# Performance work log

Hardware: AMD Instinct MI355X
Metric: run time of the kernel (lower is better)

Reference implementation:

```python
import jax, jax.numpy as jnp
import numpy as np

N_USERS = 100000
N_ITEMS = 50000
N_NODES = N_USERS + N_ITEMS
EMB_DIM = 64
N_EDGES = 4000000
N_LAYERS = 3
BATCH = 4096


def setup_inputs() -> dict:
    key = jax.random.key(0)
    k = jax.random.split(key, 7)
    return {
        "user_emb": jax.random.normal(k[0], (N_USERS, EMB_DIM), dtype=jnp.float32) * 0.1,
        "item_emb": jax.random.normal(k[1], (N_ITEMS, EMB_DIM), dtype=jnp.float32) * 0.1,
        "vals": jax.random.uniform(k[2], (N_EDGES,), dtype=jnp.float32),
        "src": jax.random.randint(k[3], (N_EDGES,), 0, N_NODES, dtype=jnp.int32),
        "dst": jax.random.randint(k[4], (N_EDGES,), 0, N_NODES, dtype=jnp.int32),
        "users": jax.random.randint(k[5], (BATCH,), 0, N_USERS, dtype=jnp.int32),
        "items": jax.random.randint(k[6], (BATCH,), 0, N_ITEMS, dtype=jnp.int32),
    }


def _propagate(user_emb, item_emb, vals, src, dst):
    # all_emb: [N, D]; sparse adjacency A given as COO (src -> dst, weight vals)
    all_emb = jnp.concatenate([user_emb, item_emb], axis=0)
    acc = all_emb  # running sum over layers (layer 0 included)
    emb = all_emb
    for _ in range(N_LAYERS):
        # SpMM: out[d] = sum_{e: dst[e]==d} vals[e] * emb[src[e]]
        msgs = vals[:, None] * emb[src]               # [E, D]
        emb = jax.ops.segment_sum(msgs, dst, num_segments=N_NODES)
        acc = acc + emb
    light_out = acc / jnp.float32(N_LAYERS + 1)       # mean over stacked layers
    return light_out[:N_USERS], light_out[N_USERS:]


def reference(user_emb, item_emb, vals, src, dst, users, items):
    all_users, all_items = _propagate(user_emb, item_emb, vals, src, dst)
    u = all_users[users]                              # [B, D]
    i = all_items[items]                              # [B, D]
    gamma = jnp.sum(u * i, axis=1)                    # [B]
    return gamma
```

## Files before the change

kernel.cpp:

```cpp
#include <hip/hip_runtime.h>
#include <hip/hip_bf16.h>

#define N_USERS 100000
#define N_ITEMS 50000
#define N_NODES 150000
#define DIM 64
#define N_EDGES 4000000
#define BATCH 4096

#define NBKT 512
#define BW 294
#define STRIDE 9216
#define PA_EDGES 4096
#define PA_ITER 16
#define SCAP 384
#define SLIST_CAP 262144

__device__ __forceinline__ float blo(unsigned int u) { return __uint_as_float(u << 16); }
__device__ __forceinline__ float bhi(unsigned int u) { return __uint_as_float(u & 0xffff0000u); }
__device__ __forceinline__ unsigned int f2b(float f) {
    unsigned int x = __float_as_uint(f);
    return (x + 0x7fffu + ((x >> 16) & 1u)) >> 16;
}
__device__ __forceinline__ unsigned int pack2(float a, float b) {
    return f2b(a) | (f2b(b) << 16);
}

typedef float v2f __attribute__((ext_vector_type(2)));

__global__ void k_markcvt(const float* __restrict__ uemb, const float* __restrict__ iemb,
                          ushort* __restrict__ out, const int* __restrict__ users,
                          const int* __restrict__ items, int* __restrict__ map,
                          int* __restrict__ sdeg, int* __restrict__ sfill,
                          int* __restrict__ gcur, int* __restrict__ scnt) {
    int tid = blockIdx.x * blockDim.x + threadIdx.x;
    if (tid < 2 * BATCH) {
        sdeg[tid] = 0;
        sfill[tid] = 0;
        if (tid < NBKT) gcur[tid] = 0;
        if (tid == 0) scnt[0] = 0;
        if (tid < BATCH) map[users[tid]] = tid;
        else map[items[tid - BATCH] + N_USERS] = tid;
    }
    int i = tid * 4;
    if (i >= N_NODES * DIM) return;
    const float* srcp = (i < N_USERS * DIM) ? (uemb + i) : (iemb + (i - N_USERS * DIM));
    float4 v;
    v.x = __builtin_nontemporal_load(srcp + 0);
    v.y = __builtin_nontemporal_load(srcp + 1);
    v.z = __builtin_nontemporal_load(srcp + 2);
    v.w = __builtin_nontemporal_load(srcp + 3);
    *(uint2*)(out + i) = make_uint2(pack2(v.x, v.y), pack2(v.z, v.w));
}

__global__ void __launch_bounds__(256, 4) k_partition(
        const int* __restrict__ src, const int* __restrict__ dst,
        const float* __restrict__ vals, const int* __restrict__ map,
        int* __restrict__ gcur, int2* __restrict__ tmp,
        int* __restrict__ sdeg, int* __restrict__ scnt,
        unsigned long long* __restrict__ slist) {
    __shared__ int cnt[NBKT];
    __shared__ int base_s[NBKT];
    __shared__ unsigned long long sbuf[SCAP];
    __shared__ int scnt_s, sbase_s;
    int t = threadIdx.x;
    for (int i = t; i < NBKT; i += 256) cnt[i] = 0;
    if (t == 0) scnt_s = 0;
    __syncthreads();
    size_t base = (size_t)blockIdx.x * PA_EDGES;
    int myb[PA_ITER];
    int mykey[PA_ITER];
    int myval[PA_ITER];
#pragma unroll
    for (int it = 0; it < PA_ITER; it++) {
        size_t i = base + (size_t)it * 256 + t;
        myb[it] = -1;
        if (i < N_EDGES) {
            int d = __builtin_nontemporal_load(dst + i);
            int s = __builtin_nontemporal_load(src + i);
            float v = __builtin_nontemporal_load(vals + i);
            int b = d / BW;
            int local = d - b * BW;
            myb[it] = b;
            mykey[it] = (s << 9) | local;
            myval[it] = __float_as_int(v);
            atomicAdd(&cnt[b], 1);
            int ms = map[d];
            if (ms >= 0) {
                atomicAdd(&sdeg[ms], 1);
                unsigned long long pk = ((unsigned long long)(unsigned int)__float_as_int(v) << 32) |
                                        ((unsigned int)ms << 18) | (unsigned int)s;
                int sl = atomicAdd(&scnt_s, 1);
                if (sl < SCAP) sbuf[sl] = pk;
                else slist[atomicAdd(scnt, 1)] = pk;
            }
        }
    }
    __syncthreads();
    for (int i = t; i < NBKT; i += 256) {
        int c = cnt[i];
        base_s[i] = (c > 0) ? atomicAdd(&gcur[i], c) : 0;
    }
    if (t == 0) {
        int c = min(scnt_s, SCAP);
        sbase_s = (c > 0) ? atomicAdd(scnt, c) : 0;
    }
    __syncthreads();
    for (int i = t; i < NBKT; i += 256) cnt[i] = 0;
    __syncthreads();
    int stot = min(scnt_s, SCAP);
    for (int i = t; i < stot; i += 256) slist[sbase_s + i] = sbuf[i];
#pragma unroll
    for (int it = 0; it < PA_ITER; it++) {
        int b = myb[it];
        if (b >= 0) {
            int pos = base_s[b] + atomicAdd(&cnt[b], 1);
            tmp[(size_t)b * STRIDE + pos] = make_int2(mykey[it], myval[it]);
        }
    }
}

__global__ void k_scan2(const int* __restrict__ gcur, int* __restrict__ bucket_ptr,
                        const int* __restrict__ sdeg, int* __restrict__ srow) {
    __shared__ int ws[16];
    int t = threadIdx.x;
    if (blockIdx.x == 0) {
        if (t >= 64) return;
        int lane = t;
        int carry = 0;
        for (int c = 0; c < NBKT / 64; c++) {
            int i = c * 64 + lane;
            int x = gcur[i];
            int incl = x;
            for (int off = 1; off < 64; off <<= 1) {
                int y = __shfl_up(incl, off);
                if (lane >= off) incl += y;
            }
            bucket_ptr[i] = carry + incl - x;
            carry += __shfl(incl, 63);
        }
        if (lane == 0) bucket_ptr[NBKT] = N_EDGES;
        return;
    }
    int v[8], p = 0;
#pragma unroll
    for (int j = 0; j < 8; j++) { v[j] = sdeg[t * 8 + j]; p += v[j]; }
    int lane = t & 63, w = t >> 6;
    int incl = p;
    for (int o = 1; o < 64; o <<= 1) {
        int y = __shfl_up(incl, o);
        if (lane >= o) incl += y;
    }
    if (lane == 63) ws[w] = incl;
    __syncthreads();
    int woff = 0;
    for (int j = 0; j < w; j++) woff += ws[j];
    int run = woff + incl - p;
#pragma unroll
    for (int j = 0; j < 8; j++) { srow[t * 8 + j] = run; run += v[j]; }
    if (t == 1023) srow[8192] = run;
}

__global__ void k_sscatter(const unsigned long long* __restrict__ slist,
                           const int* __restrict__ scnt, const int* __restrict__ srow,
                           int* __restrict__ sfill, int2* __restrict__ sfin) {
    int i = blockIdx.x * blockDim.x + threadIdx.x;
    if (i >= scnt[0]) return;
    unsigned long long pk = slist[i];
    int s = (int)(pk & 0x3FFFFu);
    int slot = (int)((pk >> 18) & 8191u);
    int vbits = (int)(pk >> 32);
    int pos = srow[slot] + atomicAdd(&sfill[slot], 1);
    sfin[pos] = make_int2(s, vbits);
}

__global__ void k_bsort(const int2* __restrict__ tmp, const int* __restrict__ gcur,
                        const int* __restrict__ bucket_ptr, int* __restrict__ row_ptr,
                        int2* __restrict__ fin) {
    __shared__ int cnt[BW + 64];
    __shared__ int off[BW + 64];
    int b = blockIdx.x, t = threadIdx.x;
    int node0 = b * BW;
    int nodes = min(BW, N_NODES - node0);
    int gbase = bucket_ptr[b];
    int count = gcur[b];
    const int2* tb = tmp + (size_t)b * STRIDE;
    for (int i = t; i < BW + 64; i += 512) cnt[i] = 0;
    __syncthreads();
    for (int e = t; e < count; e += 512) atomicAdd(&cnt[tb[e].x & 511], 1);
    __syncthreads();
    if (t < 64) {
        int lane = t;
        int carry = 0;
        for (int c = 0; c < 5; c++) {
            int i = c * 64 + lane;
            int x = (i < nodes) ? cnt[i] : 0;
            int incl = x;
            for (int o = 1; o < 64; o <<= 1) {
                int y = __shfl_up(incl, o);
                if (lane >= o) incl += y;
            }
            if (i <= nodes) off[i] = carry + incl - x;
            carry += __shfl(incl, 63);
        }
    }
    __syncthreads();
    for (int i = t; i <= nodes; i += 512)
        if (node0 + i <= N_NODES) row_ptr[node0 + i] = gbase + off[i];
    __syncthreads();
    for (int e = t; e < count; e += 512) {
        int2 r = tb[e];
        int local = r.x & 511;
        int pos = gbase + atomicAdd(&off[local], 1);
        fin[pos] = make_int2(r.x >> 9, r.y);
    }
}


#define EDGE_FMA(r, u)                                                        \
    {                                                                         \
        float vf = __int_as_float((r).y);                                     \
        v2f vv = {vf, vf};                                                    \
        v2f f0 = {blo((u).x), bhi((u).x)};                                    \
        v2f f1 = {blo((u).y), bhi((u).y)};                                    \
        v2f f2 = {blo((u).z), bhi((u).z)};                                    \
        v2f f3 = {blo((u).w), bhi((u).w)};                                    \
        acc0 = __builtin_elementwise_fma(vv, f0, acc0);                       \
        acc1 = __builtin_elementwise_fma(vv, f1, acc1);                       \
        acc2 = __builtin_elementwise_fma(vv, f2, acc2);                       \
        acc3 = __builtin_elementwise_fma(vv, f3, acc3);                       \
    }

#define GATHER16(basec, r) (*(const uint4*)((basec) + ((((unsigned int)(r).x) << 7) | qoff)))
#define REC8(basec, i) (*(const int2*)((basec) + (((unsigned int)(i)) << 3)))

#define BURST32(basec)                                                        \
    {                                                                         \
        int e1 = e + 8, e2 = e + 16, e3 = e + 24;                             \
        int2 ra = REC8(basec, e);                                             \
        int2 rb = REC8(basec, min(e1, last));                                 \
        int2 rc = REC8(basec, min(e2, last));                                 \
        int2 rd = REC8(basec, min(e3, last));                                 \
        rb.y = (e1 < end) ? rb.y : 0;                                         \
        rc.y = (e2 < end) ? rc.y : 0;                                         \
        rd.y = (e3 < end) ? rd.y : 0;                                         \
        uint4 ua = GATHER16(einc, ra);                                        \
        uint4 ub = GATHER16(einc, rb);                                        \
        uint4 uc = GATHER16(einc, rc);                                        \
        uint4 ud = GATHER16(einc, rd);                                        \
        EDGE_FMA(ra, ua);                                                     \
        EDGE_FMA(rb, ub);                                                     \
        EDGE_FMA(rc, uc);                                                     \
        EDGE_FMA(rd, ud);                                                     \
        e += 32;                                                              \
    }

__global__ void k_spmm16(const ushort* __restrict__ ein, ushort* __restrict__ eout,
                         const int* __restrict__ row_ptr, const int2* __restrict__ fin) {
    int wave = (blockIdx.x * blockDim.x + threadIdx.x) >> 6;
    if (wave >= N_NODES) return;
    int lane = threadIdx.x & 63;
    int g = lane >> 3;
    int q = lane & 7;
    unsigned int qoff = (unsigned int)q << 4;
    const char* einc = (const char*)ein;
    const char* finc = (const char*)fin;
    int start = row_ptr[wave], end = row_ptr[wave + 1];
    int last = max(start, end - 1);
    v2f acc0 = {0.f, 0.f}, acc1 = {0.f, 0.f}, acc2 = {0.f, 0.f}, acc3 = {0.f, 0.f};
    int e = start + g;
    while (e < end) BURST32(finc);
#pragma unroll
    for (int off = 8; off < 64; off <<= 1) {
        acc0.x += __shfl_xor(acc0.x, off);
        acc0.y += __shfl_xor(acc0.y, off);
        acc1.x += __shfl_xor(acc1.x, off);
        acc1.y += __shfl_xor(acc1.y, off);
        acc2.x += __shfl_xor(acc2.x, off);
        acc2.y += __shfl_xor(acc2.y, off);
        acc3.x += __shfl_xor(acc3.x, off);
        acc3.y += __shfl_xor(acc3.y, off);
    }
    if (lane < 8) {
        uint4 p;
        p.x = pack2(acc0.x, acc0.y);
        p.y = pack2(acc1.x, acc1.y);
        p.z = pack2(acc2.x, acc2.y);
        p.w = pack2(acc3.x, acc3.y);
        *(uint4*)(eout + (size_t)wave * DIM + q * 8) = p;
    }
}

__global__ void k_samp(const ushort* __restrict__ ein, const int* __restrict__ srow,
                       const int2* __restrict__ sfin, float* __restrict__ l3) {
    int slot = (blockIdx.x * blockDim.x + threadIdx.x) >> 6;
    if (slot >= 2 * BATCH) return;
    int lane = threadIdx.x & 63;
    int g = lane >> 3;
    int q = lane & 7;
    unsigned int qoff = (unsigned int)q << 4;
    const char* einc = (const char*)ein;
    const char* sfc = (const char*)sfin;
    int start = srow[slot], end = srow[slot + 1];
    int last = max(start, end - 1);
    v2f acc0 = {0.f, 0.f}, acc1 = {0.f, 0.f}, acc2 = {0.f, 0.f}, acc3 = {0.f, 0.f};
    int e = start + g;
    while (e < end) BURST32(sfc);
#pragma unroll
    for (int off = 8; off < 64; off <<= 1) {
        acc0.x += __shfl_xor(acc0.x, off);
        acc0.y += __shfl_xor(acc0.y, off);
        acc1.x += __shfl_xor(acc1.x, off);
        acc1.y += __shfl_xor(acc1.y, off);
        acc2.x += __shfl_xor(acc2.x, off);
        acc2.y += __shfl_xor(acc2.y, off);
        acc3.x += __shfl_xor(acc3.x, off);
        acc3.y += __shfl_xor(acc3.y, off);
    }
    if (lane < 8) {
        float* row = l3 + (size_t)slot * DIM + q * 8;
        *(float4*)row = make_float4(acc0.x, acc0.y, acc1.x, acc1.y);
        *(float4*)(row + 4) = make_float4(acc2.x, acc2.y, acc3.x, acc3.y);
    }
}

__global__ void k_gacc0(const float* __restrict__ uemb, const float* __restrict__ iemb,
                        const ushort* __restrict__ emb, const int* __restrict__ users,
                        const int* __restrict__ items, float* __restrict__ accU,
                        float* __restrict__ accI) {
    int i = blockIdx.x * blockDim.x + threadIdx.x;
    if (i >= 2 * BATCH * DIM) return;
    int j = (i < BATCH * DIM) ? i : i - BATCH * DIM;
    int b = j >> 6, l = j & 63;
    if (i < BATCH * DIM) {
        int n = users[b];
        unsigned int u = emb[(size_t)n * DIM + l];
        accU[j] = uemb[(size_t)n * DIM + l] + __uint_as_float(u << 16);
    } else {
        int n = items[b];
        unsigned int u = emb[(size_t)(n + N_USERS) * DIM + l];
        accI[j] = iemb[(size_t)n * DIM + l] + __uint_as_float(u << 16);
    }
}

__global__ void k_gacc(const ushort* __restrict__ emb, const int* __restrict__ users,
                       const int* __restrict__ items, float* __restrict__ accU,
                       float* __restrict__ accI) {
    int i = blockIdx.x * blockDim.x + threadIdx.x;
    if (i >= 2 * BATCH * DIM) return;
    int j = (i < BATCH * DIM) ? i : i - BATCH * DIM;
    int b = j >> 6, l = j & 63;
    if (i < BATCH * DIM) {
        unsigned int u = emb[(size_t)users[b] * DIM + l];
        accU[j] += __uint_as_float(u << 16);
    } else {
        unsigned int u = emb[(size_t)(items[b] + N_USERS) * DIM + l];
        accI[j] += __uint_as_float(u << 16);
    }
}

__global__ void k_dot(const float* __restrict__ accU, const float* __restrict__ accI,
                      const float* __restrict__ l3, const int* __restrict__ map,
                      const int* __restrict__ users, const int* __restrict__ items,
                      float* __restrict__ out) {
    int b = (blockIdx.x * blockDim.x + threadIdx.x) >> 6;
    if (b >= BATCH) return;
    int lane = threadIdx.x & 63;
    int cu = map[users[b]];
    int ci = map[items[b] + N_USERS];
    float aU = accU[b * 64 + lane] + l3[(size_t)cu * 64 + lane];
    float aI = accI[b * 64 + lane] + l3[(size_t)ci * 64 + lane];
    float p = aU * aI;
    for (int off = 32; off; off >>= 1) p += __shfl_xor(p, off);
    if (lane == 0) out[b] = p * (1.0f / 16.0f);
}


extern "C" void kernel_launch(void* const* d_in, const int* in_sizes, int n_in,
                              void* d_out, int out_size, void* d_ws, size_t ws_size,
                              hipStream_t stream) {
    const float* user_emb = (const float*)d_in[0];
    const float* item_emb = (const float*)d_in[1];
    const float* vals = (const float*)d_in[2];
    const int* src = (const int*)d_in[3];
    const int* dst = (const int*)d_in[4];
    const int* users = (const int*)d_in[5];
    const int* items = (const int*)d_in[6];
    float* out = (float*)d_out;

    char* ws = (char*)d_ws;
    size_t off = 0;
    auto alloc = [&](size_t bytes) {
        char* p = ws + off;
        off += (bytes + 255) & ~(size_t)255;
        return p;
    };
    ushort* ebf0 = (ushort*)alloc((size_t)N_NODES * DIM * 2);
    ushort* ebf1 = (ushort*)alloc((size_t)N_NODES * DIM * 2);
    ushort* ebf2 = (ushort*)alloc((size_t)N_NODES * DIM * 2);
    int2* fin = (int2*)alloc((size_t)N_EDGES * 8);
    int* row_ptr = (int*)alloc((size_t)(N_NODES + 1) * 4);
    int* bucket_ptr = (int*)alloc((size_t)(NBKT + 1) * 4);
    int* gcur = (int*)alloc((size_t)NBKT * 4);
    int* map = (int*)alloc((size_t)N_NODES * 4);
    int* sdeg = (int*)alloc((size_t)2 * BATCH * 4);
    int* srow = (int*)alloc((size_t)(2 * BATCH + 1) * 4);
    int* sfill = (int*)alloc((size_t)2 * BATCH * 4);
    int* scnt = (int*)alloc(256);
    unsigned long long* slist = (unsigned long long*)alloc((size_t)SLIST_CAP * 8);
    int2* sfin = (int2*)alloc((size_t)SLIST_CAP * 8);
    float* l3 = (float*)alloc((size_t)2 * BATCH * DIM * 4);
    float* accU = (float*)alloc((size_t)BATCH * DIM * 4);
    float* accI = (float*)alloc((size_t)BATCH * DIM * 4);
    int2* tmp = (int2*)ebf1;

    hipMemsetAsync(map, 0xFF, (size_t)N_NODES * 4, stream);

    k_markcvt<<<(N_NODES * DIM / 4 + 255) / 256, 256, 0, stream>>>(
        user_emb, item_emb, ebf0, users, items, map, sdeg, sfill, gcur, scnt);

    int pa_blocks = (N_EDGES + PA_EDGES - 1) / PA_EDGES;
    k_partition<<<pa_blocks, 256, 0, stream>>>(src, dst, vals, map, gcur, tmp, sdeg, scnt, slist);
    k_scan2<<<2, 1024, 0, stream>>>(gcur, bucket_ptr, sdeg, srow);
    k_sscatter<<<SLIST_CAP / 256, 256, 0, stream>>>(slist, scnt, srow, sfill, sfin);
    k_bsort<<<NBKT, 512, 0, stream>>>(tmp, gcur, bucket_ptr, row_ptr, fin);

    int gb = (2 * BATCH * DIM + 255) / 256;
    int spmm_blocks = (N_NODES * 64 + 255) / 256;
    k_spmm16<<<spmm_blocks, 256, 0, stream>>>(ebf0, ebf1, row_ptr, fin);
    k_gacc0<<<gb, 256, 0, stream>>>(user_emb, item_emb, ebf1, users, items, accU, accI);
    k_spmm16<<<spmm_blocks, 256, 0, stream>>>(ebf1, ebf2, row_ptr, fin);
    k_gacc<<<gb, 256, 0, stream>>>(ebf2, users, items, accU, accI);
    k_samp<<<(2 * BATCH * 64 + 255) / 256, 256, 0, stream>>>(ebf2, srow, sfin, l3);

    k_dot<<<(BATCH * 64 + 255) / 256, 256, 0, stream>>>(accU, accI, l3, map, users, items, out);
}
```

Baseline: 382.2 us.

## Drop sampled-row side list; stage partition writes in LDS for coalesced scatter

Removes the separate map/sdeg/slist/sscatter machinery that built a private CSR for the batch's sampled nodes. The final-layer sample kernel now reads the batch rows directly from the global CSR (row_ptr/fin). This eliminates a memset, the per-edge map lookups and atomics, and two kernel launches. The partition kernel also locally sorts each block's edges by bucket in shared memory and writes them out contiguously per bucket, which should make the global scatter writes more coalesced. The cost is more LDS per block (about 45KB), which may reduce occupancy.

```diff
diff --git a/kernel.cpp b/kernel.cpp
--- a/kernel.cpp
+++ b/kernel.cpp
@@ -13,8 +13,6 @@
 #define STRIDE 9216
 #define PA_EDGES 4096
 #define PA_ITER 16
-#define SCAP 384
-#define SLIST_CAP 262144
 
 __device__ __forceinline__ float blo(unsigned int u) { return __uint_as_float(u << 16); }
 __device__ __forceinline__ float bhi(unsigned int u) { return __uint_as_float(u & 0xffff0000u); }
@@ -29,19 +27,9 @@
 typedef float v2f __attribute__((ext_vector_type(2)));
 
 __global__ void k_markcvt(const float* __restrict__ uemb, const float* __restrict__ iemb,
-                          ushort* __restrict__ out, const int* __restrict__ users,
-                          const int* __restrict__ items, int* __restrict__ map,
-                          int* __restrict__ sdeg, int* __restrict__ sfill,
-                          int* __restrict__ gcur, int* __restrict__ scnt) {
+                          ushort* __restrict__ out, int* __restrict__ gcur) {
     int tid = blockIdx.x * blockDim.x + threadIdx.x;
-    if (tid < 2 * BATCH) {
-        sdeg[tid] = 0;
-        sfill[tid] = 0;
-        if (tid < NBKT) gcur[tid] = 0;
-        if (tid == 0) scnt[0] = 0;
-        if (tid < BATCH) map[users[tid]] = tid;
-        else map[items[tid - BATCH] + N_USERS] = tid;
-    }
+    if (tid < NBKT) gcur[tid] = 0;
     int i = tid * 4;
     if (i >= N_NODES * DIM) return;
     const float* srcp = (i < N_USERS * DIM) ? (uemb + i) : (iemb + (i - N_USERS * DIM));
@@ -55,17 +43,15 @@
 
 __global__ void __launch_bounds__(256, 4) k_partition(
         const int* __restrict__ src, const int* __restrict__ dst,
-        const float* __restrict__ vals, const int* __restrict__ map,
-        int* __restrict__ gcur, int2* __restrict__ tmp,
-        int* __restrict__ sdeg, int* __restrict__ scnt,
-        unsigned long long* __restrict__ slist) {
+        const float* __restrict__ vals,
+        int* __restrict__ gcur, int2* __restrict__ tmp) {
     __shared__ int cnt[NBKT];
     __shared__ int base_s[NBKT];
-    __shared__ unsigned long long sbuf[SCAP];
-    __shared__ int scnt_s, sbase_s;
+    __shared__ int off_s[NBKT];
+    __shared__ int2 rec_s[PA_EDGES];
+    __shared__ ushort bin_s[PA_EDGES];
     int t = threadIdx.x;
     for (int i = t; i < NBKT; i += 256) cnt[i] = 0;
-    if (t == 0) scnt_s = 0;
     __syncthreads();
     size_t base = (size_t)blockIdx.x * PA_EDGES;
     int myb[PA_ITER];
@@ -85,15 +71,6 @@
             mykey[it] = (s << 9) | local;
             myval[it] = __float_as_int(v);
             atomicAdd(&cnt[b], 1);
-            int ms = map[d];
-            if (ms >= 0) {
-                atomicAdd(&sdeg[ms], 1);
-                unsigned long long pk = ((unsigned long long)(unsigned int)__float_as_int(v) << 32) |
-                                        ((unsigned int)ms << 18) | (unsigned int)s;
-                int sl = atomicAdd(&scnt_s, 1);
-                if (sl < SCAP) sbuf[sl] = pk;
-                else slist[atomicAdd(scnt, 1)] = pk;
-            }
         }
     }
     __syncthreads();
@@ -101,77 +78,57 @@
         int c = cnt[i];
         base_s[i] = (c > 0) ? atomicAdd(&gcur[i], c) : 0;
     }
-    if (t == 0) {
-        int c = min(scnt_s, SCAP);
-        sbase_s = (c > 0) ? atomicAdd(scnt, c) : 0;
+    if (t < 64) {
+        int lane = t;
+        int carry = 0;
+        for (int c = 0; c < NBKT / 64; c++) {
+            int i = c * 64 + lane;
+            int x = cnt[i];
+            int incl = x;
+            for (int o = 1; o < 64; o <<= 1) {
+                int y = __shfl_up(incl, o);
+                if (lane >= o) incl += y;
+            }
+            off_s[i] = carry + incl - x;
+            carry += __shfl(incl, 63);
+        }
     }
     __syncthreads();
     for (int i = t; i < NBKT; i += 256) cnt[i] = 0;
     __syncthreads();
-    int stot = min(scnt_s, SCAP);
-    for (int i = t; i < stot; i += 256) slist[sbase_s + i] = sbuf[i];
 #pragma unroll
     for (int it = 0; it < PA_ITER; it++) {
         int b = myb[it];
         if (b >= 0) {
-            int pos = base_s[b] + atomicAdd(&cnt[b], 1);
-            tmp[(size_t)b * STRIDE + pos] = make_int2(mykey[it], myval[it]);
-        }
-    }
-}
-
-__global__ void k_scan2(const int* __restrict__ gcur, int* __restrict__ bucket_ptr,
-                        const int* __restrict__ sdeg, int* __restrict__ srow) {
-    __shared__ int ws[16];
-    int t = threadIdx.x;
-    if (blockIdx.x == 0) {
-        if (t >= 64) return;
-        int lane = t;
-        int carry = 0;
-        for (int c = 0; c < NBKT / 64; c++) {
-            int i = c * 64 + lane;
-            int x = gcur[i];
-            int incl = x;
-            for (int off = 1; off < 64; off <<= 1) {
-                int y = __shfl_up(incl, off);
-                if (lane >= off) incl += y;
-            }
-            bucket_ptr[i] = carry + incl - x;
-            carry += __shfl(incl, 63);
-        }
-        if (lane == 0) bucket_ptr[NBKT] = N_EDGES;
-        return;
-    }
-    int v[8], p = 0;
-#pragma unroll
-    for (int j = 0; j < 8; j++) { v[j] = sdeg[t * 8 + j]; p += v[j]; }
-    int lane = t & 63, w = t >> 6;
-    int incl = p;
-    for (int o = 1; o < 64; o <<= 1) {
-        int y = __shfl_up(incl, o);
-        if (lane >= o) incl += y;
-    }
-    if (lane == 63) ws[w] = incl;
-    __syncthreads();
-    int woff = 0;
-    for (int j = 0; j < w; j++) woff += ws[j];
-    int run = woff + incl - p;
-#pragma unroll
-    for (int j = 0; j < 8; j++) { srow[t * 8 + j] = run; run += v[j]; }
-    if (t == 1023) srow[8192] = run;
-}
-
-__global__ void k_sscatter(const unsigned long long* __restrict__ slist,
-                           const int* __restrict__ scnt, const int* __restrict__ srow,
-                           int* __restrict__ sfill, int2* __restrict__ sfin) {
-    int i = blockIdx.x * blockDim.x + threadIdx.x;
-    if (i >= scnt[0]) return;
-    unsigned long long pk = slist[i];
-    int s = (int)(pk & 0x3FFFFu);
-    int slot = (int)((pk >> 18) & 8191u);
-    int vbits = (int)(pk >> 32);
-    int pos = srow[slot] + atomicAdd(&sfill[slot], 1);
-    sfin[pos] = make_int2(s, vbits);
+            int pos = off_s[b] + atomicAdd(&cnt[b], 1);
+            rec_s[pos] = make_int2(mykey[it], myval[it]);
+            bin_s[pos] = (ushort)b;
+        }
+    }
+    __syncthreads();
+    int nrec = off_s[NBKT - 1] + cnt[NBKT - 1];
+    for (int i = t; i < nrec; i += 256) {
+        int2 r = rec_s[i];
+        int b = bin_s[i];
+        tmp[(size_t)b * STRIDE + base_s[b] + (i - off_s[b])] = r;
+    }
+}
+
+__global__ void k_scan(const int* __restrict__ gcur, int* __restrict__ bucket_ptr) {
+    int lane = threadIdx.x;
+    int carry = 0;
+    for (int c = 0; c < NBKT / 64; c++) {
+        int i = c * 64 + lane;
+        int x = gcur[i];
+        int incl = x;
+        for (int off = 1; off < 64; off <<= 1) {
+            int y = __shfl_up(incl, off);
+            if (lane >= off) incl += y;
+        }
+        bucket_ptr[i] = carry + incl - x;
+        carry += __shfl(incl, 63);
+    }
+    if (lane == 0) bucket_ptr[NBKT] = N_EDGES;
 }
 
 __global__ void k_bsort(const int2* __restrict__ tmp, const int* __restrict__ gcur,
@@ -291,8 +248,9 @@
     }
 }
 
-__global__ void k_samp(const ushort* __restrict__ ein, const int* __restrict__ srow,
-                       const int2* __restrict__ sfin, float* __restrict__ l3) {
+__global__ void k_samp(const ushort* __restrict__ ein, const int* __restrict__ row_ptr,
+                       const int2* __restrict__ fin, const int* __restrict__ users,
+                       const int* __restrict__ items, float* __restrict__ l3) {
     int slot = (blockIdx.x * blockDim.x + threadIdx.x) >> 6;
     if (slot >= 2 * BATCH) return;
     int lane = threadIdx.x & 63;
@@ -300,12 +258,13 @@
     int q = lane & 7;
     unsigned int qoff = (unsigned int)q << 4;
     const char* einc = (const char*)ein;
-    const char* sfc = (const char*)sfin;
-    int start = srow[slot], end = srow[slot + 1];
+    const char* finc = (const char*)fin;
+    int node = (slot < BATCH) ? users[slot] : (items[slot - BATCH] + N_USERS);
+    int start = row_ptr[node], end = row_ptr[node + 1];
     int last = max(start, end - 1);
     v2f acc0 = {0.f, 0.f}, acc1 = {0.f, 0.f}, acc2 = {0.f, 0.f}, acc3 = {0.f, 0.f};
     int e = start + g;
-    while (e < end) BURST32(sfc);
+    while (e < end) BURST32(finc);
 #pragma unroll
     for (int off = 8; off < 64; off <<= 1) {
         acc0.x += __shfl_xor(acc0.x, off);
@@ -360,16 +319,12 @@
 }
 
 __global__ void k_dot(const float* __restrict__ accU, const float* __restrict__ accI,
-                      const float* __restrict__ l3, const int* __restrict__ map,
-                      const int* __restrict__ users, const int* __restrict__ items,
-                      float* __restrict__ out) {
+                      const float* __restrict__ l3, float* __restrict__ out) {
     int b = (blockIdx.x * blockDim.x + threadIdx.x) >> 6;
     if (b >= BATCH) return;
     int lane = threadIdx.x & 63;
-    int cu = map[users[b]];
-    int ci = map[items[b] + N_USERS];
-    float aU = accU[b * 64 + lane] + l3[(size_t)cu * 64 + lane];
-    float aI = accI[b * 64 + lane] + l3[(size_t)ci * 64 + lane];
+    float aU = accU[b * 64 + lane] + l3[(size_t)b * 64 + lane];
+    float aI = accI[b * 64 + lane] + l3[(size_t)(BATCH + b) * 64 + lane];
     float p = aU * aI;
     for (int off = 32; off; off >>= 1) p += __shfl_xor(p, off);
     if (lane == 0) out[b] = p * (1.0f / 16.0f);
@@ -402,27 +357,17 @@
     int* row_ptr = (int*)alloc((size_t)(N_NODES + 1) * 4);
     int* bucket_ptr = (int*)alloc((size_t)(NBKT + 1) * 4);
     int* gcur = (int*)alloc((size_t)NBKT * 4);
-    int* map = (int*)alloc((size_t)N_NODES * 4);
-    int* sdeg = (int*)alloc((size_t)2 * BATCH * 4);
-    int* srow = (int*)alloc((size_t)(2 * BATCH + 1) * 4);
-    int* sfill = (int*)alloc((size_t)2 * BATCH * 4);
-    int* scnt = (int*)alloc(256);
-    unsigned long long* slist = (unsigned long long*)alloc((size_t)SLIST_CAP * 8);
-    int2* sfin = (int2*)alloc((size_t)SLIST_CAP * 8);
     float* l3 = (float*)alloc((size_t)2 * BATCH * DIM * 4);
     float* accU = (float*)alloc((size_t)BATCH * DIM * 4);
     float* accI = (float*)alloc((size_t)BATCH * DIM * 4);
     int2* tmp = (int2*)ebf1;
 
-    hipMemsetAsync(map, 0xFF, (size_t)N_NODES * 4, stream);
-
     k_markcvt<<<(N_NODES * DIM / 4 + 255) / 256, 256, 0, stream>>>(
-        user_emb, item_emb, ebf0, users, items, map, sdeg, sfill, gcur, scnt);
+        user_emb, item_emb, ebf0, gcur);
 
     int pa_blocks = (N_EDGES + PA_EDGES - 1) / PA_EDGES;
-    k_partition<<<pa_blocks, 256, 0, stream>>>(src, dst, vals, map, gcur, tmp, sdeg, scnt, slist);
-    k_scan2<<<2, 1024, 0, stream>>>(gcur, bucket_ptr, sdeg, srow);
-    k_sscatter<<<SLIST_CAP / 256, 256, 0, stream>>>(slist, scnt, srow, sfill, sfin);
+    k_partition<<<pa_blocks, 256, 0, stream>>>(src, dst, vals, gcur, tmp);
+    k_scan<<<1, 64, 0, stream>>>(gcur, bucket_ptr);
     k_bsort<<<NBKT, 512, 0, stream>>>(tmp, gcur, bucket_ptr, row_ptr, fin);
 
     int gb = (2 * BATCH * DIM + 255) / 256;
@@ -431,7 +376,7 @@
     k_gacc0<<<gb, 256, 0, stream>>>(user_emb, item_emb, ebf1, users, items, accU, accI);
     k_spmm16<<<spmm_blocks, 256, 0, stream>>>(ebf1, ebf2, row_ptr, fin);
     k_gacc<<<gb, 256, 0, stream>>>(ebf2, users, items, accU, accI);
-    k_samp<<<(2 * BATCH * 64 + 255) / 256, 256, 0, stream>>>(ebf2, srow, sfin, l3);
-
-    k_dot<<<(BATCH * 64 + 255) / 256, 256, 0, stream>>>(accU, accI, l3, map, users, items, out);
-}
+    k_samp<<<(2 * BATCH * 64 + 255) / 256, 256, 0, stream>>>(ebf2, row_ptr, fin, users, items, l3);
+
+    k_dot<<<(BATCH * 64 + 255) / 256, 256, 0, stream>>>(accU, accI, l3, out);
+}
```

After: 342.5 us. -10.4%, faster.
